# Optimization experiments

Hardware: AMD Instinct MI355X
Metric: run time of the kernel (lower is better)

The kernel has to match this reference:

```python
import jax, jax.numpy as jnp
import numpy as np

NUM_CLASSES = 19
EPS = 1e-8  # torch cosine_similarity eps


def setup_inputs() -> dict:
    key = jax.random.key(0)
    k1, k2 = jax.random.split(key)
    inputs = jax.random.normal(k1, (8, 256, 128, 128), dtype=jnp.float32)  # (B, D, H, W)
    targets = jax.random.randint(k2, (8, 128, 128), 0, NUM_CLASSES)        # (B, H, W)
    return {"inputs": inputs, "targets": targets}


def reference(inputs, targets):
    B, D, H, W = inputs.shape
    C = NUM_CLASSES
    # (N, D) pixel embeddings and (N,) labels
    feats = jnp.transpose(inputs, (0, 2, 3, 1)).reshape(-1, D)
    labels = targets.reshape(-1)

    # per-class centroids: sum of embeddings / max(count, 1)  (matches sum_pixel = max(mask.sum(), 1))
    counts = jax.ops.segment_sum(jnp.ones(labels.shape, jnp.float32), labels, num_segments=C)  # (C,)
    sums = jax.ops.segment_sum(feats, labels, num_segments=C)                                   # (C, D)
    centers = sums / jnp.maximum(counts, 1.0)[:, None]
    present = counts > 0  # classes absent from the batch are skipped in both loss terms

    # ---- sim_loss: sum over present classes of mean_{pixels of class i} (1 - cos(center_i, feat)) ----
    cen_px = centers[labels]                                   # (N, D)
    dot = jnp.sum(feats * cen_px, axis=1)
    n_f = jnp.sqrt(jnp.sum(feats * feats, axis=1))
    n_c = jnp.sqrt(jnp.sum(cen_px * cen_px, axis=1))
    cos_px = dot / jnp.maximum(n_f * n_c, EPS)
    per_class = jax.ops.segment_sum(1.0 - cos_px, labels, num_segments=C) / jnp.maximum(counts, 1.0)
    sim_loss = jnp.sum(jnp.where(present, per_class, 0.0))

    # ---- diff_loss: for each present i, mean_j over all C classes of
    #      (1 - cos(center_j, center_i)) if j == i else relu(cos(center_j, center_i)) ----
    n_cen = jnp.sqrt(jnp.sum(centers * centers, axis=1))       # (C,)
    S = (centers @ centers.T) / jnp.maximum(n_cen[:, None] * n_cen[None, :], EPS)  # (C, C)
    eye = jnp.eye(C, dtype=bool)
    per_pair = jnp.where(eye, 1.0 - S, jnp.maximum(S, 0.0))    # row i = losses vs class i
    per_i = jnp.mean(per_pair, axis=1)                          # mean reduction over C rows
    diff_loss = jnp.sum(jnp.where(present, per_i, 0.0))

    return jnp.reshape(diff_loss + sim_loss, (1,))  # torch returns a shape-(1,) tensor
```

## Files before the change

### kernel.cpp

```cpp
#include <hip/hip_runtime.h>
#include <math.h>

#define D_DIM 256
#define HW 16384
#define C 19
#define N_PX 131072
#define EPS 1e-8f

#define S_SC  1048576.0f
#define IS_S  (1.0f/1048576.0f)
#define U_SC  16777216.0f
#define IS_U  (1.0f/16777216.0f)

#define OFF_S    0
#define OFF_U    4864
#define OFF_CNT  9728
#define WS_ZERO  9760
#define OFF_PART 9760
#define PSTRIDE  9760
#define G1       512

__global__ __launch_bounds__(512, 4) void k1_pass(const float* __restrict__ in,
                                                  const int* __restrict__ tgt,
                                                  int* __restrict__ wsi) {
    __shared__ int sS[C * 257];
    __shared__ int sU[C * 257];
    __shared__ int s_cnt[C];
    __shared__ float s_nfp[128 * 9];
    const int tid = threadIdx.x;
    const int w   = tid >> 6;
    const int ln  = tid & 63;

    for (int i = tid; i < C * 257; i += 512) { sS[i] = 0; sU[i] = 0; }
    if (tid < C) s_cnt[tid] = 0;
    if (blockIdx.x < 20) {
        int i = (blockIdx.x << 9) + tid;
        if (i < WS_ZERO) wsi[i] = 0;
    }
    __syncthreads();

    const int px0 = blockIdx.x << 8;
    const int b   = px0 >> 14;
    const float* bbase = in + (((size_t)(b * D_DIM + (w << 5))) << 14)
                            + (px0 & (HW - 1));

    #pragma unroll
    for (int r = 0; r < 2; ++r) {
        const int pp = (r << 7) + (ln << 1);
        const int2 lab = *(const int2*)(tgt + px0 + pp);
        const int la = lab.x, lb = lab.y;
        if (w == 0) { atomicAdd(&s_cnt[la], 1); atomicAdd(&s_cnt[lb], 1); }

        float2 v[32];
        #pragma unroll
        for (int cc = 0; cc < 32; ++cc)
            v[cc] = *(const float2*)(bbase + ((size_t)cc << 14) + pp);

        const int rowa = la * 257, rowb = lb * 257;

        #pragma unroll
        for (int cc = 0; cc < 32; ++cc) {
            const int dd = (w << 5) + cc;
            atomicAdd(&sS[rowa + dd], __float2int_rn(v[cc].x * S_SC));
            atomicAdd(&sS[rowb + dd], __float2int_rn(v[cc].y * S_SC));
        }

        float na = 0.f, nb = 0.f;
        #pragma unroll
        for (int cc = 0; cc < 32; ++cc) {
            na += v[cc].x * v[cc].x;
            nb += v[cc].y * v[cc].y;
        }
        s_nfp[(pp - (r << 7)) * 9 + w]     = na;
        s_nfp[(pp - (r << 7) + 1) * 9 + w] = nb;
        __syncthreads();
        float sumA = 0.f, sumB = 0.f;
        #pragma unroll
        for (int ww = 0; ww < 8; ++ww) {
            sumA += s_nfp[(ln << 1) * 9 + ww];
            sumB += ((ln << 1) + 1) * 9 + ww >= 0 ? s_nfp[((ln << 1) + 1) * 9 + ww] : 0.f;
        }
        const float sa = sumA > 0.f ? U_SC / sqrtf(sumA) : 0.f;
        const float sb = sumB > 0.f ? U_SC / sqrtf(sumB) : 0.f;

        #pragma unroll
        for (int cc = 0; cc < 32; ++cc) {
            const int dd = (w << 5) + cc;
            atomicAdd(&sU[rowa + dd], __float2int_rn(v[cc].x * sa));
            atomicAdd(&sU[rowb + dd], __float2int_rn(v[cc].y * sb));
        }
        __syncthreads();
    }

    int* __restrict__ row = wsi + OFF_PART + (size_t)blockIdx.x * PSTRIDE;
    for (int i = tid; i < C * 256; i += 512) {
        int c = i >> 8, d = i & 255;
        row[OFF_S + i] = sS[c * 257 + d];
        row[OFF_U + i] = sU[c * 257 + d];
    }
    if (tid < C)                 row[OFF_CNT + tid] = s_cnt[tid];
    else if (tid < 32)           row[OFF_CNT + tid] = 0;
}

__global__ __launch_bounds__(256) void k1b_reduce(int* __restrict__ wsi) {
    const int col4 = blockIdx.x * 256 + threadIdx.x;
    if (col4 >= PSTRIDE / 4) return;
    const int4* base = (const int4*)(wsi + OFF_PART)
                     + (size_t)blockIdx.y * 16 * (PSTRIDE / 4) + col4;
    int4 acc = {0, 0, 0, 0};
    #pragma unroll
    for (int r = 0; r < 16; ++r) {
        int4 v = base[(size_t)r * (PSTRIDE / 4)];
        acc.x += v.x; acc.y += v.y; acc.z += v.z; acc.w += v.w;
    }
    atomicAdd(&wsi[col4 * 4 + 0], acc.x);
    atomicAdd(&wsi[col4 * 4 + 1], acc.y);
    atomicAdd(&wsi[col4 * 4 + 2], acc.z);
    atomicAdd(&wsi[col4 * 4 + 3], acc.w);
}

__global__ __launch_bounds__(512) void k2_final(const int* __restrict__ wsi,
                                                float* __restrict__ out) {
    __shared__ __align__(16) float s_cen[C * 260];
    __shared__ __align__(16) float s_u[C * 260];
    __shared__ float s_nc[C];
    __shared__ float s_cntf[C];
    __shared__ float s_pair[C * C];
    __shared__ float s_sim[C];
    const int tid = threadIdx.x;

    if (tid < C) s_cntf[tid] = (float)wsi[OFF_CNT + tid];
    __syncthreads();
    for (int i = tid; i < C * 256; i += 512) {
        int c = i >> 8, d = i & 255;
        float icnt = 1.f / fmaxf(s_cntf[c], 1.f);
        s_cen[c * 260 + d] = (float)wsi[OFF_S + i] * IS_S * icnt;
        s_u[c * 260 + d]   = (float)wsi[OFF_U + i] * IS_U;
    }
    __syncthreads();
    if (tid < C) {
        float nsq = 0.f;
        for (int d = 0; d < D_DIM; ++d) {
            float x = s_cen[tid * 260 + d];
            nsq += x * x;
        }
        s_nc[tid] = sqrtf(nsq);
    }
    __syncthreads();
    if (tid < C * C) {
        int i = tid / C, j = tid % C;
        const float4* ci = (const float4*)&s_cen[i * 260];
        const float4* cj = (const float4*)&s_cen[j * 260];
        float dot = 0.f;
        #pragma unroll 8
        for (int k = 0; k < 64; ++k) {
            float4 a = ci[k], bb = cj[k];
            dot += a.x * bb.x + a.y * bb.y + a.z * bb.z + a.w * bb.w;
        }
        float S = dot / fmaxf(s_nc[i] * s_nc[j], EPS);
        s_pair[tid] = (i == j) ? (1.f - S) : fmaxf(S, 0.f);
    } else if (tid >= 384 && tid < 384 + C) {
        int i = tid - 384;
        const float4* ci = (const float4*)&s_cen[i * 260];
        const float4* ui = (const float4*)&s_u[i * 260];
        float dot = 0.f;
        #pragma unroll 8
        for (int k = 0; k < 64; ++k) {
            float4 a = ci[k], bb = ui[k];
            dot += a.x * bb.x + a.y * bb.y + a.z * bb.z + a.w * bb.w;
        }
        s_sim[i] = (s_cntf[i] > 0.f)
                 ? (1.f - dot / fmaxf(s_nc[i] * s_cntf[i], EPS)) : 0.f;
    }
    __syncthreads();
    if (tid < C) {
        float row = 0.f;
        for (int j = 0; j < C; ++j) row += s_pair[tid * C + j];
        s_pair[tid * C] = (s_cntf[tid] > 0.f) ? (row * (1.f / (float)C)) : 0.f;
    }
    __syncthreads();
    if (tid == 0) {
        float tot = 0.f;
        for (int i = 0; i < C; ++i) tot += s_pair[i * C] + s_sim[i];
        out[0] = tot;
    }
}

extern "C" void kernel_launch(void* const* d_in, const int* in_sizes, int n_in,
                              void* d_out, int out_size, void* d_ws, size_t ws_size,
                              hipStream_t stream) {
    const float* in  = (const float*)d_in[0];
    const int*   tgt = (const int*)d_in[1];
    float* out = (float*)d_out;
    int*   wsi = (int*)d_ws;

    k1_pass<<<G1, 512, 0, stream>>>(in, tgt, wsi);
    k1b_reduce<<<dim3(10, 32), 256, 0, stream>>>(wsi);
    k2_final<<<1, 512, 0, stream>>>(wsi, out);
}
```

Before: 224.0 us.

## Transpose pixel tiles through LDS so atomics hit distinct channels per wave

The main loop now processes 32-pixel tiles. Each tile is loaded as float4 along pixels, transposed into an LDS tile, and then scattered with one wave per pixel and lanes spanning channels. Before, each wave issued atomics where all 64 lanes targeted the same channel in a few class rows, so the LDS atomics conflicted heavily. Lanes now hit consecutive addresses in a single row. In exchange, the pixel-norm reduction moves to cross-lane shuffles, there are more tile iterations and barriers, LDS use grows, and the occupancy hint drops from 4 to 2 blocks.

```diff
diff --git a/kernel.cpp b/kernel.cpp
--- a/kernel.cpp
+++ b/kernel.cpp
@@ -19,17 +19,23 @@
 #define OFF_PART 9760
 #define PSTRIDE  9760
 #define G1       512
-
-__global__ __launch_bounds__(512, 4) void k1_pass(const float* __restrict__ in,
+#define TPX      32
+
+__global__ __launch_bounds__(512, 2) void k1_pass(const float* __restrict__ in,
                                                   const int* __restrict__ tgt,
                                                   int* __restrict__ wsi) {
-    __shared__ int sS[C * 257];
-    __shared__ int sU[C * 257];
-    __shared__ int s_cnt[C];
-    __shared__ float s_nfp[128 * 9];
+    __shared__ int   sS[C * 257];
+    __shared__ int   sU[C * 257];
+    __shared__ int   s_cnt[C];
+    __shared__ float ldsT[TPX * 257];
+    __shared__ float s_nfp[TPX * 9];
+    __shared__ float s_scale[TPX];
+    __shared__ int   s_lab[TPX];
     const int tid = threadIdx.x;
     const int w   = tid >> 6;
     const int ln  = tid & 63;
+    const int lg  = ln >> 3;
+    const int pxo = (ln & 7) << 2;
 
     for (int i = tid; i < C * 257; i += 512) { sS[i] = 0; sU[i] = 0; }
     if (tid < C) s_cnt[tid] = 0;
@@ -41,53 +47,71 @@
 
     const int px0 = blockIdx.x << 8;
     const int b   = px0 >> 14;
-    const float* bbase = in + (((size_t)(b * D_DIM + (w << 5))) << 14)
-                            + (px0 & (HW - 1));
-
-    #pragma unroll
-    for (int r = 0; r < 2; ++r) {
-        const int pp = (r << 7) + (ln << 1);
-        const int2 lab = *(const int2*)(tgt + px0 + pp);
-        const int la = lab.x, lb = lab.y;
-        if (w == 0) { atomicAdd(&s_cnt[la], 1); atomicAdd(&s_cnt[lb], 1); }
-
-        float2 v[32];
-        #pragma unroll
-        for (int cc = 0; cc < 32; ++cc)
-            v[cc] = *(const float2*)(bbase + ((size_t)cc << 14) + pp);
-
-        const int rowa = la * 257, rowb = lb * 257;
-
-        #pragma unroll
-        for (int cc = 0; cc < 32; ++cc) {
-            const int dd = (w << 5) + cc;
-            atomicAdd(&sS[rowa + dd], __float2int_rn(v[cc].x * S_SC));
-            atomicAdd(&sS[rowb + dd], __float2int_rn(v[cc].y * S_SC));
-        }
-
-        float na = 0.f, nb = 0.f;
-        #pragma unroll
-        for (int cc = 0; cc < 32; ++cc) {
-            na += v[cc].x * v[cc].x;
-            nb += v[cc].y * v[cc].y;
-        }
-        s_nfp[(pp - (r << 7)) * 9 + w]     = na;
-        s_nfp[(pp - (r << 7) + 1) * 9 + w] = nb;
+
+    #pragma unroll 1
+    for (int t = 0; t < 8; ++t) {
+        const int P  = px0 + (t << 5);
+        const int hw = (P & (HW - 1)) + pxo;
+
+        if (tid < TPX) {
+            const int lab = tgt[P + tid];
+            s_lab[tid] = lab;
+            atomicAdd(&s_cnt[lab], 1);
+        }
+        float4 v[4];
+        #pragma unroll
+        for (int g = 0; g < 4; ++g) {
+            const int pl = (w << 5) + (g << 3) + lg;
+            v[g] = *(const float4*)(in + (((size_t)(b * D_DIM + pl)) << 14) + hw);
+        }
+        #pragma unroll
+        for (int g = 0; g < 4; ++g) {
+            const int pl = (w << 5) + (g << 3) + lg;
+            ldsT[(pxo + 0) * 257 + pl] = v[g].x;
+            ldsT[(pxo + 1) * 257 + pl] = v[g].y;
+            ldsT[(pxo + 2) * 257 + pl] = v[g].z;
+            ldsT[(pxo + 3) * 257 + pl] = v[g].w;
+        }
+        float n0 = v[0].x*v[0].x + v[1].x*v[1].x + v[2].x*v[2].x + v[3].x*v[3].x;
+        float n1 = v[0].y*v[0].y + v[1].y*v[1].y + v[2].y*v[2].y + v[3].y*v[3].y;
+        float n2 = v[0].z*v[0].z + v[1].z*v[1].z + v[2].z*v[2].z + v[3].z*v[3].z;
+        float n3 = v[0].w*v[0].w + v[1].w*v[1].w + v[2].w*v[2].w + v[3].w*v[3].w;
+        #pragma unroll
+        for (int m = 8; m <= 32; m <<= 1) {
+            n0 += __shfl_xor(n0, m, 64);
+            n1 += __shfl_xor(n1, m, 64);
+            n2 += __shfl_xor(n2, m, 64);
+            n3 += __shfl_xor(n3, m, 64);
+        }
+        if (lg == 0) {
+            s_nfp[(pxo + 0) * 9 + w] = n0;
+            s_nfp[(pxo + 1) * 9 + w] = n1;
+            s_nfp[(pxo + 2) * 9 + w] = n2;
+            s_nfp[(pxo + 3) * 9 + w] = n3;
+        }
         __syncthreads();
-        float sumA = 0.f, sumB = 0.f;
-        #pragma unroll
-        for (int ww = 0; ww < 8; ++ww) {
-            sumA += s_nfp[(ln << 1) * 9 + ww];
-            sumB += ((ln << 1) + 1) * 9 + ww >= 0 ? s_nfp[((ln << 1) + 1) * 9 + ww] : 0.f;
-        }
-        const float sa = sumA > 0.f ? U_SC / sqrtf(sumA) : 0.f;
-        const float sb = sumB > 0.f ? U_SC / sqrtf(sumB) : 0.f;
-
-        #pragma unroll
-        for (int cc = 0; cc < 32; ++cc) {
-            const int dd = (w << 5) + cc;
-            atomicAdd(&sU[rowa + dd], __float2int_rn(v[cc].x * sa));
-            atomicAdd(&sU[rowb + dd], __float2int_rn(v[cc].y * sb));
+
+        if (tid < TPX) {
+            float nf = 0.f;
+            #pragma unroll
+            for (int ww = 0; ww < 8; ++ww) nf += s_nfp[tid * 9 + ww];
+            s_scale[tid] = nf > 0.f ? U_SC / sqrtf(nf) : 0.f;
+        }
+        __syncthreads();
+
+        #pragma unroll
+        for (int k = 0; k < 4; ++k) {
+            const int   lp  = (w << 2) + k;
+            const int   lab = s_lab[lp];
+            const float sc  = s_scale[lp];
+            const int   rowc = lab * 257;
+            #pragma unroll
+            for (int g2 = 0; g2 < 4; ++g2) {
+                const int   ch  = (g2 << 6) + ln;
+                const float val = ldsT[lp * 257 + ch];
+                atomicAdd(&sS[rowc + ch], __float2int_rn(val * S_SC));
+                atomicAdd(&sU[rowc + ch], __float2int_rn(val * sc));
+            }
         }
         __syncthreads();
     }
```

Measured after the change: 216.2 us. 3.5% less time.
